# Kernel optimization log

Measured on AMD Instinct MI355X. Metric: run time of the kernel, lower is better.

Reference implementation:

```python
import jax, jax.numpy as jnp
import numpy as np

# Model dims
B, S, H, NH = 2, 2048, 1024, 8
HD = H // NH            # head_dim = 128
T = S * NH              # MoE input tokens per batch = 16384
E, K, F = 8, 2, 512     # experts, top_k, expert FFN dim (4*head_dim)


def setup_inputs() -> dict:
    key = jax.random.key(0)
    ks = jax.random.split(key, 9)
    s = 0.02  # init scale
    return {
        "x": jax.random.normal(ks[0], (B, S, H), jnp.float32),
        "W_mh": jax.random.normal(ks[1], (H, H), jnp.float32) * s,
        "b_mh": jnp.zeros((H,), jnp.float32),
        "W_merge": jax.random.normal(ks[2], (H, H), jnp.float32) * s,
        "b_merge": jnp.zeros((H,), jnp.float32),
        "W_router": jax.random.normal(ks[3], (HD, E), jnp.float32) * s,
        "W1": jax.random.normal(ks[4], (E, HD, F), jnp.float32) * s,
        "b1": jnp.zeros((E, F), jnp.float32),
        "W2": jax.random.normal(ks[5], (E, F, HD), jnp.float32) * s,
        "b2": jnp.zeros((E, HD), jnp.float32),
    }


def reference(x, W_mh, b_mh, W_merge, b_merge, W_router, W1, b1, W2, b2):
    # multi-head projection then split heads into the token axis
    h = x @ W_mh + b_mh                       # [B, S, H]
    h = h.reshape(B, T, HD)                   # [B, T, HD]

    # nested VectorizedMoE: top-k token-choice routing over head_dim tokens
    logits = h @ W_router                     # [B, T, E]
    probs = jax.nn.softmax(logits, axis=-1)
    topv, topi = jax.lax.top_k(probs, K)      # [B, T, K]
    topv = topv / jnp.sum(topv, axis=-1, keepdims=True)  # renormalize top-k gates
    # scatter top-k gates into dense [B, T, E] combine weights
    gates = jnp.sum(jax.nn.one_hot(topi, E, dtype=h.dtype) * topv[..., None], axis=-2)

    # vectorized expert FFNs (all experts, combined with sparse gates)
    a = jax.nn.gelu(jnp.einsum('btd,edf->btef', h, W1) + b1)   # [B, T, E, F]
    y = jnp.einsum('btef,efd->bted', a, W2) + b2               # [B, T, E, HD]
    moe_out = jnp.einsum('bte,bted->btd', gates, y)            # [B, T, HD]

    # merge heads back and final projection
    out = moe_out.reshape(B, S, H) @ W_merge + b_merge         # [B, S, H]
    return out
```

## Files before the change

### kernel.cpp

```cpp
#include <hip/hip_runtime.h>


typedef __attribute__((ext_vector_type(8))) short bf16x8;
typedef __attribute__((ext_vector_type(4))) float f32x4;
typedef __attribute__((ext_vector_type(16))) float f32x16;
typedef __attribute__((ext_vector_type(4))) unsigned short u16x4;

constexpr int NSLOT = 66560;
constexpr int NTILE_MAX = 520;
#define CTRL_CNT 0
#define CTRL_CUR 8

__device__ __forceinline__ unsigned short f2bf(float x) {
  unsigned int u = __float_as_uint(x);
  return (unsigned short)((u + 0x7FFFu + ((u >> 16) & 1u)) >> 16);
}
__device__ __forceinline__ float bf2f(unsigned short u) {
  return __uint_as_float(((unsigned int)u) << 16);
}
__device__ __forceinline__ void gload_lds16(const void* g, void* l) {
  __builtin_amdgcn_global_load_lds(
      (const __attribute__((address_space(1))) unsigned int*)g,
      (__attribute__((address_space(3))) unsigned int*)l, 16, 0, 0);
}

__global__ __launch_bounds__(256) void prep_all(
    const float* __restrict__ Wmh, unsigned short* __restrict__ Wmh_t,
    const float* __restrict__ Wmg, unsigned short* __restrict__ Wmg_t,
    const float* __restrict__ W1, const float* __restrict__ W2,
    unsigned short* __restrict__ W1F, unsigned short* __restrict__ W2F,
    const float* __restrict__ bmh, const float* __restrict__ Wr,
    float* __restrict__ Wc, int* __restrict__ ctrl) {
  __shared__ float smem[2048];
  const int bid = blockIdx.x, tid = threadIdx.x;
  if (bid < 2048) {
    if (bid == 0 && tid < 16) ctrl[tid] = 0;
    const float* src = (bid < 1024) ? Wmh : Wmg;
    unsigned short* dst = (bid < 1024) ? Wmh_t : Wmg_t;
    const int bb = bid & 1023;
    const int c0 = (bb & 31) * 32, r0 = (bb >> 5) * 32;
    const int tx = tid & 31, ty = tid >> 5;
    float (*tile)[33] = (float(*)[33])smem;
    for (int i = ty; i < 32; i += 8)
      tile[i][tx] = src[(size_t)(r0 + i) * 1024 + c0 + tx];
    __syncthreads();
    for (int i = ty; i < 32; i += 8)
      dst[(size_t)(c0 + i) * 1024 + r0 + tx] = f2bf(tile[tx][i]);
  } else if (bid < 2560) {
    const int jid = (bid - 2048) * 4 + (tid >> 6);
    const int l = tid & 63;
    const int is2 = jid >= 1024;
    const int bj = is2 ? jid - 1024 : jid;
    const float* src;
    int C;
    if (!is2) {
      int kk = bj & 7, ft = (bj >> 3) & 15, e = bj >> 7;
      src = W1 + (size_t)e * 65536 + (size_t)(kk * 16) * 512 + ft * 32;
      C = 512;
    } else {
      int sht = bj & 7, ft = (bj >> 3) & 15, e = bj >> 7;
      src = W2 + (size_t)e * 65536 + (size_t)(ft * 32 + (sht >> 2) * 16) * 128 + (sht & 3) * 32;
      C = 128;
    }
    float* tile = smem + (tid >> 6) * 512;
#pragma unroll
    for (int r = 0; r < 8; ++r) {
      int i = l + 64 * r;
      tile[(i >> 5) * 32 + (i & 31)] = src[(size_t)(i >> 5) * C + (i & 31)];
    }
    __syncthreads();
    int l31 = l & 31, lh = l >> 5;
    bf16x8 v;
#pragma unroll
    for (int j = 0; j < 8; ++j) v[j] = (short)f2bf(tile[(lh * 8 + j) * 32 + l31]);
    unsigned short* dst = is2 ? W2F : W1F;
    *(bf16x8*)(dst + ((size_t)bj * 64 + l) * 8) = v;
  } else {
    const int r = (bid - 2560) * 4 + (tid >> 6);
    if (r > 1024) return;
    const int l = tid & 63;
    const float* src = (r < 1024) ? (Wmh + (size_t)r * 1024) : bmh;
    int nh = l >> 3, e = l & 7;
    float acc = 0.f;
    for (int d = 0; d < 128; ++d) acc = fmaf(src[nh * 128 + d], Wr[d * 8 + e], acc);
    Wc[(size_t)r * 64 + l] = acc;
  }
}

__global__ __launch_bounds__(256) void router_kernel(
    const float* __restrict__ x, const float* __restrict__ Wc,
    int* __restrict__ tok_e, float* __restrict__ tok_g,
    int* __restrict__ ctrl, int* __restrict__ perm, float* __restrict__ gateb,
    unsigned short* __restrict__ x_bf) {
  const int tid = threadIdx.x;
  int gi = blockIdx.x * 256 + tid;
  if (gi < NSLOT) { perm[gi] = 0; gateb[gi] = 0.f; }

  __shared__ float lg[8][64];
  __shared__ int lcnt[8];
  if (tid < 8) lcnt[tid] = 0;
  const int r0 = blockIdx.x * 8;
  const int lane = tid & 63;

  if (tid < 128) {
    const int wr = __builtin_amdgcn_readfirstlane(tid >> 6);
    const float* xrow = x + (size_t)(r0 + wr * 4) * 1024;
    float a0 = Wc[65536 + lane];
    float a1 = a0, a2 = a0, a3 = a0;
    for (int k = 0; k < 1024; k += 8) {
      float xv0[8], xv1[8], xv2[8], xv3[8];
#pragma unroll
      for (int u = 0; u < 8; ++u) {
        xv0[u] = xrow[k + u];
        xv1[u] = xrow[1024 + k + u];
        xv2[u] = xrow[2048 + k + u];
        xv3[u] = xrow[3072 + k + u];
      }
#pragma unroll
      for (int u = 0; u < 8; ++u) {
        float wv = Wc[(size_t)(k + u) * 64 + lane];
        a0 = fmaf(xv0[u], wv, a0);
        a1 = fmaf(xv1[u], wv, a1);
        a2 = fmaf(xv2[u], wv, a2);
        a3 = fmaf(xv3[u], wv, a3);
      }
    }
    lg[wr * 4 + 0][lane] = a0;
    lg[wr * 4 + 1][lane] = a1;
    lg[wr * 4 + 2][lane] = a2;
    lg[wr * 4 + 3][lane] = a3;
  } else {
    const int ct = tid - 128;
    const float4* xg = (const float4*)(x + (size_t)r0 * 1024);
    u16x4* xb4 = (u16x4*)(x_bf + (size_t)r0 * 1024);
    for (int i = ct; i < 2048; i += 128) {
      float4 v = xg[i];
      u16x4 o;
      o.x = f2bf(v.x); o.y = f2bf(v.y); o.z = f2bf(v.z); o.w = f2bf(v.w);
      xb4[i] = o;
    }
  }
  __syncthreads();
  if (tid < 64) {
    int row = tid >> 3, nh = tid & 7;
    float l[8];
#pragma unroll
    for (int e = 0; e < 8; ++e) l[e] = lg[row][nh * 8 + e];
    int i1 = 0; float v1 = l[0];
#pragma unroll
    for (int e = 1; e < 8; ++e) if (l[e] > v1) { v1 = l[e]; i1 = e; }
    int i2 = -1; float v2 = -1e30f;
#pragma unroll
    for (int e = 0; e < 8; ++e) if (e != i1 && l[e] > v2) { v2 = l[e]; i2 = e; }
    float g1 = 1.f / (1.f + __expf(v2 - v1));
    float g2 = 1.f - g1;
    size_t t = (size_t)(r0 + row) * 8 + nh;
    tok_e[t * 2] = i1; tok_e[t * 2 + 1] = i2;
    tok_g[t * 2] = g1; tok_g[t * 2 + 1] = g2;
    atomicAdd(&lcnt[i1], 1);
    atomicAdd(&lcnt[i2], 1);
  }
  __syncthreads();
  if (tid < 8 && lcnt[tid])
    atomicAdd(&ctrl[CTRL_CNT + tid], lcnt[tid]);
}

__global__ __launch_bounds__(256) void assign_kernel(
    const int* __restrict__ tok_e, const float* __restrict__ tok_g,
    int* __restrict__ ctrl, int* __restrict__ perm,
    float* __restrict__ gateb, int* __restrict__ tok_slot) {
  __shared__ int lcnt[8], lbase[8];
  if (threadIdx.x < 8) lcnt[threadIdx.x] = 0;
  __syncthreads();
  int t = blockIdx.x * 256 + threadIdx.x;
  int e0 = tok_e[t * 2], e1 = tok_e[t * 2 + 1];
  int p0 = atomicAdd(&lcnt[e0], 1);
  int p1 = atomicAdd(&lcnt[e1], 1);
  __syncthreads();
  if (threadIdx.x < 8)
    lbase[threadIdx.x] = atomicAdd(&ctrl[CTRL_CUR + threadIdx.x], lcnt[threadIdx.x]);
  __syncthreads();
  int off0 = 0, off1 = 0, acc = 0;
#pragma unroll
  for (int i = 0; i < 8; ++i) {
    int cnt = ctrl[CTRL_CNT + i];
    if (i == e0) off0 = acc;
    if (i == e1) off1 = acc;
    acc += (cnt + 127) & ~127;
  }
  int s0 = off0 + lbase[e0] + p0;
  int s1 = off1 + lbase[e1] + p1;
  perm[s0] = t; perm[s1] = t;
  gateb[s0] = tok_g[t * 2]; gateb[s1] = tok_g[t * 2 + 1];
  tok_slot[t * 2] = s0; tok_slot[t * 2 + 1] = s1;
}

template <int OUT_BF16, int A_GATHER>
__global__ __launch_bounds__(512, 4) void gemm_bt(
    const unsigned short* __restrict__ A, const unsigned short* __restrict__ Bt,
    const float* __restrict__ bias, void* __restrict__ Cout,
    int M, int N, int K,
    const unsigned short* __restrict__ ybuf, const int* __restrict__ tok_slot) {
  __shared__ __align__(16) unsigned short As[2][128 * 64];
  __shared__ __align__(16) unsigned short Bs[2][128 * 64];
  const int tid = threadIdx.x, lane = tid & 63, w = tid >> 6;
  const int wr = w >> 1, wc = w & 1;
  const int m0 = blockIdx.x * 128, n0 = blockIdx.y * 128;
  const int l15 = lane & 15, lhi = lane >> 4;

  f32x4 acc[2][4];
#pragma unroll
  for (int n = 0; n < 4; ++n) {
    float bv = bias[n0 + wc * 64 + n * 16 + l15];
#pragma unroll
    for (int m = 0; m < 2; ++m) acc[m][n] = (f32x4){bv, bv, bv, bv};
  }

  const int rowi = tid >> 3;
  const int segi = (tid & 7) * 8;
  const int NT = K >> 6;

  auto stage = [&](int buf, int kt) {
    const int k0 = kt * 64;
    if constexpr (A_GATHER) {
#pragma unroll
      for (int r = 0; r < 2; ++r) {
        int arow = m0 + r * 64 + rowi;
        int k = k0 + segi;
        int tok = arow * 8 + (k >> 7);
        int hd = k & 127;
        int s0 = tok_slot[tok * 2], s1 = tok_slot[tok * 2 + 1];
        bf16x8 va = *(const bf16x8*)(ybuf + (size_t)s0 * 128 + hd);
        bf16x8 vb = *(const bf16x8*)(ybuf + (size_t)s1 * 128 + hd);
        bf16x8 vs;
#pragma unroll
        for (int j = 0; j < 8; ++j)
          vs[j] = (short)f2bf(bf2f((unsigned short)va[j]) + bf2f((unsigned short)vb[j]));
        *(bf16x8*)&As[buf][r * 4096 + tid * 8] = vs;
      }
    } else {
#pragma unroll
      for (int r = 0; r < 2; ++r)
        gload_lds16(A + (size_t)(m0 + r * 64 + rowi) * K + k0 + segi,
                    &As[buf][r * 4096 + w * 512]);
    }
#pragma unroll
    for (int r = 0; r < 2; ++r)
      gload_lds16(Bt + (size_t)(n0 + r * 64 + rowi) * K + k0 + segi,
                  &Bs[buf][r * 4096 + w * 512]);
  };

  stage(0, 0);
  asm volatile("s_waitcnt vmcnt(0)" ::: "memory");
  __syncthreads();
  int cur = 0;
  for (int t = 0; t < NT; ++t) {
    if (t + 1 < NT) stage(cur ^ 1, t + 1);
#pragma unroll
    for (int ks = 0; ks < 64; ks += 32) {
      bf16x8 af[2], bb[4];
#pragma unroll
      for (int m = 0; m < 2; ++m)
        af[m] = *(const bf16x8*)&As[cur][(wr * 32 + m * 16 + l15) * 64 + ks + lhi * 8];
#pragma unroll
      for (int n = 0; n < 4; ++n)
        bb[n] = *(const bf16x8*)&Bs[cur][(wc * 64 + n * 16 + l15) * 64 + ks + lhi * 8];
#pragma unroll
      for (int m = 0; m < 2; ++m)
#pragma unroll
        for (int n = 0; n < 4; ++n)
          acc[m][n] = __builtin_amdgcn_mfma_f32_16x16x32_bf16(af[m], bb[n], acc[m][n], 0, 0, 0);
    }
    asm volatile("s_waitcnt vmcnt(0)" ::: "memory");
    __syncthreads();
    cur ^= 1;
  }
#pragma unroll
  for (int m = 0; m < 2; ++m) {
#pragma unroll
    for (int n = 0; n < 4; ++n) {
      int col = n0 + wc * 64 + n * 16 + l15;
#pragma unroll
      for (int j = 0; j < 4; ++j) {
        int row = m0 + wr * 32 + m * 16 + lhi * 4 + j;
        if (OUT_BF16)
          ((unsigned short*)Cout)[(size_t)row * N + col] = f2bf(acc[m][n][j]);
        else
          ((float*)Cout)[(size_t)row * N + col] = acc[m][n][j];
      }
    }
  }
}

__global__ __launch_bounds__(256, 2) void ffn_sparse_v3(
    const unsigned short* __restrict__ hbf,
    const int* __restrict__ ctrl,
    const int* __restrict__ perm,
    const float* __restrict__ gateb,
    const unsigned short* __restrict__ W1F,
    const float* __restrict__ b1,
    const unsigned short* __restrict__ W2F,
    const float* __restrict__ b2,
    unsigned short* __restrict__ ybuf) {
  int e = -1;
  {
    int accT = 0;
#pragma unroll
    for (int i = 0; i < 8; ++i) {
      int tiles = (ctrl[CTRL_CNT + i] + 127) >> 7;
      if (e < 0 && (int)blockIdx.x < accT + tiles) e = i;
      accT += tiles;
    }
  }
  if (e < 0) return;
  __shared__ unsigned short W1c[2][4096];
  __shared__ unsigned short W2c[2][4096];
  __shared__ float b1_s[512];
  __shared__ float b2_s[128];
  const int tid = threadIdx.x, l = tid & 63, w = tid >> 6;
  const int l31 = l & 31, lh = l >> 5;
  const int slot = blockIdx.x * 128 + w * 32 + l31;
  const int prow = perm[slot];
  const float gate = gateb[slot];

  bf16x8 hreg[8];
  const unsigned short* hsrc = hbf + (size_t)prow * 128 + lh * 8;
#pragma unroll
  for (int kk = 0; kk < 8; ++kk)
    hreg[kk] = *(const bf16x8*)(hsrc + kk * 16);

  if (tid < 128) ((float4*)b1_s)[tid] = ((const float4*)(b1 + e * 512))[tid];
  if (tid < 32)  ((float4*)b2_s)[tid] = ((const float4*)(b2 + e * 128))[tid];

  const unsigned short* W1e = W1F + (size_t)e * 65536;
  const unsigned short* W2e = W2F + (size_t)e * 65536;
  auto stage = [&](int buf, int ft) {
#pragma unroll
    for (int r = 0; r < 2; ++r) {
      gload_lds16(W1e + (size_t)ft * 4096 + (size_t)(r * 256 + tid) * 8,
                  &W1c[buf][r * 2048 + w * 512]);
      gload_lds16(W2e + (size_t)ft * 4096 + (size_t)(r * 256 + tid) * 8,
                  &W2c[buf][r * 2048 + w * 512]);
    }
  };

  stage(0, 0);
  asm volatile("s_waitcnt vmcnt(0)" ::: "memory");
  __syncthreads();

  f32x16 yacc[4] = {};
  int cur = 0;
  for (int ft = 0; ft < 16; ++ft) {
    if (ft < 15) stage(cur ^ 1, ft + 1);
    const float4* b14 = (const float4*)b1_s;
    float4 q0 = b14[ft * 8 + lh];
    float4 q1 = b14[ft * 8 + lh + 2];
    float4 q2 = b14[ft * 8 + lh + 4];
    float4 q3 = b14[ft * 8 + lh + 6];
    f32x16 aacc = {q0.x, q0.y, q0.z, q0.w, q1.x, q1.y, q1.z, q1.w,
                   q2.x, q2.y, q2.z, q2.w, q3.x, q3.y, q3.z, q3.w};
#pragma unroll
    for (int kk = 0; kk < 8; ++kk) {
      bf16x8 a1 = *(const bf16x8*)&W1c[cur][(kk * 64 + l) * 8];
      aacc = __builtin_amdgcn_mfma_f32_32x32x16_bf16(a1, hreg[kk], aacc, 0, 0, 0);
    }
    float ge[16];
#pragma unroll
    for (int r = 0; r < 16; ++r) {
      float v = aacc[r];
      float s2 = v * v;
      float q = fmaf(0.1029432f, s2, 2.3022078f);
      float E = exp2f(v * q);
      float rc = __builtin_amdgcn_rcpf(E + 1.f);
      ge[r] = fmaf(-v, rc, v) * gate;
    }
    unsigned pk[8];
#pragma unroll
    for (int p = 0; p < 8; ++p) {
      unsigned r;
      asm("v_cvt_pk_bf16_f32 %0, %1, %2" : "=v"(r) : "v"(ge[2 * p]), "v"(ge[2 * p + 1]));
      pk[p] = r;
    }
    asm volatile("v_permlane32_swap_b32 %0, %1" : "+v"(pk[0]), "+v"(pk[2]));
    asm volatile("v_permlane32_swap_b32 %0, %1" : "+v"(pk[1]), "+v"(pk[3]));
    asm volatile("v_permlane32_swap_b32 %0, %1" : "+v"(pk[4]), "+v"(pk[6]));
    asm volatile("v_permlane32_swap_b32 %0, %1" : "+v"(pk[5]), "+v"(pk[7]));
    typedef __attribute__((ext_vector_type(4))) unsigned u32x4;
    u32x4 f0 = {pk[0], pk[1], pk[2], pk[3]};
    u32x4 f1 = {pk[4], pk[5], pk[6], pk[7]};
    bf16x8 act0 = __builtin_bit_cast(bf16x8, f0);
    bf16x8 act1 = __builtin_bit_cast(bf16x8, f1);
#pragma unroll
    for (int ht = 0; ht < 4; ++ht) {
      bf16x8 a20 = *(const bf16x8*)&W2c[cur][(ht * 64 + l) * 8];
      yacc[ht] = __builtin_amdgcn_mfma_f32_32x32x16_bf16(a20, act0, yacc[ht], 0, 0, 0);
      bf16x8 a21 = *(const bf16x8*)&W2c[cur][((4 + ht) * 64 + l) * 8];
      yacc[ht] = __builtin_amdgcn_mfma_f32_32x32x16_bf16(a21, act1, yacc[ht], 0, 0, 0);
    }
    asm volatile("s_waitcnt vmcnt(0)" ::: "memory");
    __syncthreads();
    cur ^= 1;
  }
#pragma unroll
  for (int ht = 0; ht < 4; ++ht) {
#pragma unroll
    for (int rp = 0; rp < 8; ++rp) {
      int fr = ((2 * rp) & 3) + 8 * (rp >> 1) + 4 * lh;
      int hd = ht * 32 + fr;
      float2 bb2 = *(const float2*)&b2_s[hd];
      float v0 = fmaf(gate, bb2.x, yacc[ht][2 * rp]);
      float v1 = fmaf(gate, bb2.y, yacc[ht][2 * rp + 1]);
      unsigned pw;
      asm("v_cvt_pk_bf16_f32 %0, %1, %2" : "=v"(pw) : "v"(v0), "v"(v1));
      *(unsigned*)(ybuf + (size_t)slot * 128 + hd) = pw;
    }
  }
}

extern "C" void kernel_launch(void* const* d_in, const int* in_sizes, int n_in,
                              void* d_out, int out_size, void* d_ws, size_t ws_size,
                              hipStream_t stream) {
  const float* x       = (const float*)d_in[0];
  const float* W_mh    = (const float*)d_in[1];
  const float* b_mh    = (const float*)d_in[2];
  const float* W_merge = (const float*)d_in[3];
  const float* b_merge = (const float*)d_in[4];
  const float* W_rout  = (const float*)d_in[5];
  const float* W1      = (const float*)d_in[6];
  const float* b1      = (const float*)d_in[7];
  const float* W2      = (const float*)d_in[8];
  const float* b2      = (const float*)d_in[9];
  float* out = (float*)d_out;

  char* ws = (char*)d_ws;
  size_t off = 0;
  auto alloc = [&](size_t bytes) {
    void* p = ws + off;
    off = (off + bytes + 255) & ~(size_t)255;
    return p;
  };
  unsigned short* x_bf  = (unsigned short*)alloc((size_t)4096 * 1024 * 2);
  unsigned short* Wmh_t = (unsigned short*)alloc((size_t)1024 * 1024 * 2);
  unsigned short* Wmg_t = (unsigned short*)alloc((size_t)1024 * 1024 * 2);
  unsigned short* W1F   = (unsigned short*)alloc((size_t)8 * 512 * 128 * 2);
  unsigned short* W2F   = (unsigned short*)alloc((size_t)8 * 512 * 128 * 2);
  unsigned short* h_bf  = (unsigned short*)alloc((size_t)4096 * 1024 * 2);
  unsigned short* ybuf  = (unsigned short*)alloc((size_t)NSLOT * 128 * 2);
  float* Wc             = (float*)alloc((size_t)1025 * 64 * 4);
  int*   ctrl           = (int*)alloc(4096);
  int*   tok_e          = (int*)alloc((size_t)32768 * 2 * 4);
  float* tok_g          = (float*)alloc((size_t)32768 * 2 * 4);
  int*   tok_slot       = (int*)alloc((size_t)32768 * 2 * 4);
  int*   perm           = (int*)alloc((size_t)NSLOT * 4);
  float* gateb          = (float*)alloc((size_t)NSLOT * 4);

  prep_all<<<2817, 256, 0, stream>>>(W_mh, Wmh_t, W_merge, Wmg_t,
                                     W1, W2, W1F, W2F, b_mh, W_rout, Wc, ctrl);
  router_kernel<<<512, 256, 0, stream>>>(x, Wc, tok_e, tok_g, ctrl, perm, gateb, x_bf);
  assign_kernel<<<128, 256, 0, stream>>>(tok_e, tok_g, ctrl, perm, gateb, tok_slot);
  gemm_bt<1, 0><<<dim3(32, 8), 512, 0, stream>>>(x_bf, Wmh_t, b_mh, (void*)h_bf,
                                                 4096, 1024, 1024, nullptr, nullptr);
  ffn_sparse_v3<<<NTILE_MAX, 256, 0, stream>>>(h_bf, ctrl, perm, gateb, W1F, b1, W2F, b2, ybuf);
  gemm_bt<0, 1><<<dim3(32, 8), 512, 0, stream>>>(nullptr, Wmg_t, b_merge, (void*)out,
                                                 4096, 1024, 1024, ybuf, tok_slot);
}
```

Baseline: 162.6 us.

## Split router logits into K-chunked partial GEMV and separate reduce kernel

The router logit computation, previously done by 512 blocks each streaming a full 1024-wide row range with only half the threads doing math, is split into a split-K partial kernel (8 K-chunks × 128 row blocks) that stages x and the combined router weights in LDS, plus a reduce kernel that sums the partials and does top-2 selection. The partial kernel also performs the bf16 conversion of x and the perm/gate zeroing. This is meant to raise parallelism and reuse for the router stage. In exchange it adds an 8 MB partial buffer round trip through memory and one extra kernel launch.

```diff
diff --git a/kernel.cpp b/kernel.cpp
--- a/kernel.cpp
+++ b/kernel.cpp
@@ -87,61 +87,74 @@
   }
 }
 
-__global__ __launch_bounds__(256) void router_kernel(
+__global__ __launch_bounds__(256) void router_partial(
     const float* __restrict__ x, const float* __restrict__ Wc,
+    float* __restrict__ part, unsigned short* __restrict__ x_bf,
+    int* __restrict__ perm, float* __restrict__ gateb) {
+  const int tid = threadIdx.x;
+  const int kc = blockIdx.x, rb = blockIdx.y;
+  int gi = (rb * 8 + kc) * 256 + tid;
+  if (gi < NSLOT) { perm[gi] = 0; gateb[gi] = 0.f; }
+
+  __shared__ float xs[32][128];
+  __shared__ float wcs[128][64];
+  const int r0 = rb * 32, k0 = kc * 128;
+
+  for (int f = tid; f < 1024; f += 256) {
+    int row = f >> 5, j4 = (f & 31) * 4;
+    float4 v = *(const float4*)&x[(size_t)(r0 + row) * 1024 + k0 + j4];
+    *(float4*)&xs[row][j4] = v;
+    u16x4 o;
+    o.x = f2bf(v.x); o.y = f2bf(v.y); o.z = f2bf(v.z); o.w = f2bf(v.w);
+    *(u16x4*)&x_bf[(size_t)(r0 + row) * 1024 + k0 + j4] = o;
+  }
+  {
+    const float4* src = (const float4*)(Wc + (size_t)k0 * 64);
+    float4* dst = (float4*)&wcs[0][0];
+    for (int f = tid; f < 2048; f += 256) dst[f] = src[f];
+  }
+  __syncthreads();
+
+  const int col = tid & 63, rg = tid >> 6;
+  float a[8] = {0.f, 0.f, 0.f, 0.f, 0.f, 0.f, 0.f, 0.f};
+  for (int k4 = 0; k4 < 32; ++k4) {
+    float4 xv[8];
+#pragma unroll
+    for (int i = 0; i < 8; ++i)
+      xv[i] = *(const float4*)&xs[rg * 8 + i][k4 * 4];
+#pragma unroll
+    for (int u = 0; u < 4; ++u) {
+      float wv = wcs[k4 * 4 + u][col];
+#pragma unroll
+      for (int i = 0; i < 8; ++i)
+        a[i] = fmaf((&xv[i].x)[u], wv, a[i]);
+    }
+  }
+#pragma unroll
+  for (int i = 0; i < 8; ++i)
+    part[(size_t)kc * 262144 + (size_t)(r0 + rg * 8 + i) * 64 + col] = a[i];
+}
+
+__global__ __launch_bounds__(256) void router_reduce(
+    const float* __restrict__ part, const float* __restrict__ Wc,
     int* __restrict__ tok_e, float* __restrict__ tok_g,
-    int* __restrict__ ctrl, int* __restrict__ perm, float* __restrict__ gateb,
-    unsigned short* __restrict__ x_bf) {
+    int* __restrict__ ctrl) {
+  __shared__ float lg[32][64];
+  __shared__ int lcnt[8];
   const int tid = threadIdx.x;
-  int gi = blockIdx.x * 256 + tid;
-  if (gi < NSLOT) { perm[gi] = 0; gateb[gi] = 0.f; }
-
-  __shared__ float lg[8][64];
-  __shared__ int lcnt[8];
   if (tid < 8) lcnt[tid] = 0;
-  const int r0 = blockIdx.x * 8;
-  const int lane = tid & 63;
-
-  if (tid < 128) {
-    const int wr = __builtin_amdgcn_readfirstlane(tid >> 6);
-    const float* xrow = x + (size_t)(r0 + wr * 4) * 1024;
-    float a0 = Wc[65536 + lane];
-    float a1 = a0, a2 = a0, a3 = a0;
-    for (int k = 0; k < 1024; k += 8) {
-      float xv0[8], xv1[8], xv2[8], xv3[8];
-#pragma unroll
-      for (int u = 0; u < 8; ++u) {
-        xv0[u] = xrow[k + u];
-        xv1[u] = xrow[1024 + k + u];
-        xv2[u] = xrow[2048 + k + u];
-        xv3[u] = xrow[3072 + k + u];
-      }
-#pragma unroll
-      for (int u = 0; u < 8; ++u) {
-        float wv = Wc[(size_t)(k + u) * 64 + lane];
-        a0 = fmaf(xv0[u], wv, a0);
-        a1 = fmaf(xv1[u], wv, a1);
-        a2 = fmaf(xv2[u], wv, a2);
-        a3 = fmaf(xv3[u], wv, a3);
-      }
-    }
-    lg[wr * 4 + 0][lane] = a0;
-    lg[wr * 4 + 1][lane] = a1;
-    lg[wr * 4 + 2][lane] = a2;
-    lg[wr * 4 + 3][lane] = a3;
-  } else {
-    const int ct = tid - 128;
-    const float4* xg = (const float4*)(x + (size_t)r0 * 1024);
-    u16x4* xb4 = (u16x4*)(x_bf + (size_t)r0 * 1024);
-    for (int i = ct; i < 2048; i += 128) {
-      float4 v = xg[i];
-      u16x4 o;
-      o.x = f2bf(v.x); o.y = f2bf(v.y); o.z = f2bf(v.z); o.w = f2bf(v.w);
-      xb4[i] = o;
-    }
-  }
-  __syncthreads();
-  if (tid < 64) {
+  const int r0 = blockIdx.x * 32;
+  const int col = tid & 63, rg = tid >> 6;
+#pragma unroll
+  for (int i = 0; i < 8; ++i) {
+    size_t base = (size_t)(r0 + rg * 8 + i) * 64 + col;
+    float s = Wc[65536 + col];
+#pragma unroll
+    for (int kc = 0; kc < 8; ++kc) s += part[(size_t)kc * 262144 + base];
+    lg[rg * 8 + i][col] = s;
+  }
+  __syncthreads();
+  {
     int row = tid >> 3, nh = tid & 7;
     float l[8];
 #pragma unroll
@@ -447,6 +460,7 @@
   unsigned short* h_bf  = (unsigned short*)alloc((size_t)4096 * 1024 * 2);
   unsigned short* ybuf  = (unsigned short*)alloc((size_t)NSLOT * 128 * 2);
   float* Wc             = (float*)alloc((size_t)1025 * 64 * 4);
+  float* part           = (float*)alloc((size_t)8 * 4096 * 64 * 4);
   int*   ctrl           = (int*)alloc(4096);
   int*   tok_e          = (int*)alloc((size_t)32768 * 2 * 4);
   float* tok_g          = (float*)alloc((size_t)32768 * 2 * 4);
@@ -456,7 +470,8 @@
 
   prep_all<<<2817, 256, 0, stream>>>(W_mh, Wmh_t, W_merge, Wmg_t,
                                      W1, W2, W1F, W2F, b_mh, W_rout, Wc, ctrl);
-  router_kernel<<<512, 256, 0, stream>>>(x, Wc, tok_e, tok_g, ctrl, perm, gateb, x_bf);
+  router_partial<<<dim3(8, 128), 256, 0, stream>>>(x, Wc, part, x_bf, perm, gateb);
+  router_reduce<<<128, 256, 0, stream>>>(part, Wc, tok_e, tok_g, ctrl);
   assign_kernel<<<128, 256, 0, stream>>>(tok_e, tok_g, ctrl, perm, gateb, tok_slot);
   gemm_bt<1, 0><<<dim3(32, 8), 512, 0, stream>>>(x_bf, Wmh_t, b_mh, (void*)h_bf,
                                                  4096, 1024, 1024, nullptr, nullptr);
```

After: 139.3 us. -14.3%, faster.
